# Kernel optimization log

Measured on AMD Instinct MI355X. Metric: run time of the kernel, lower is better.

## Reference

```python
import jax, jax.numpy as jnp
import numpy as np

D_ATT = 1024
N_HEADS = 16
D_HEAD = D_ATT // N_HEADS


def _xavier(key, shape, scale):
    # xavier_uniform for Linear(d, d): limit = sqrt(6/(fan_in+fan_out))
    limit = float(np.sqrt(6.0 / (shape[0] + shape[1])))
    return jax.random.uniform(key, shape, jnp.float32, -limit, limit) * scale


def setup_inputs() -> dict:
    key = jax.random.key(0)
    ks = jax.random.split(key, 7)
    B, Lt, Ls = 2, 2048, 2048
    s = 1.0 / np.sqrt(D_ATT)
    return {
        "x_target": jax.random.normal(ks[0], (B, Lt, D_ATT), jnp.float32),
        "x_source": jax.random.normal(ks[1], (B, Ls, D_ATT), jnp.float32),
        "Wq": _xavier(ks[2], (D_ATT, D_ATT), s),  # torch Linear weight [out, in]
        "Wk": _xavier(ks[3], (D_ATT, D_ATT), s),
        "Wv": _xavier(ks[4], (D_ATT, D_ATT), s),
        "Wo": _xavier(ks[5], (D_ATT, D_ATT), 1.0),
        "bo": jax.random.uniform(ks[6], (D_ATT,), jnp.float32, -s, s),
    }


def reference(x_target, x_source, Wq, Wk, Wv, Wo, bo):
    B, Lt, _ = x_target.shape
    Ls = x_source.shape[1]
    H, Dh = N_HEADS, D_HEAD
    # projections (torch Linear: x @ W^T); RoPE defaults to identity
    Q = (x_target @ Wq.T).reshape(B, Lt, H, Dh)  # [B, Lt, H, Dh]
    K = (x_source @ Wk.T).reshape(B, Ls, H, Dh)
    V = (x_source @ Wv.T).reshape(B, Ls, H, Dh)
    scores = jnp.einsum("bthd,bshd->bhts", Q, K) / np.sqrt(Dh)
    attn = jax.nn.softmax(scores, axis=-1)
    out = jnp.einsum("bhts,bshd->bthd", attn, V).reshape(B, Lt, H * Dh)
    return out @ Wo.T + bo  # dropout p=0 -> identity
```

## Files before the change

kernel.cpp:

```cpp
#include <hip/hip_runtime.h>
#include <hip/hip_bf16.h>

typedef short bf16x8 __attribute__((ext_vector_type(8)));
typedef float f32x4 __attribute__((ext_vector_type(4)));
typedef unsigned int uint2v __attribute__((ext_vector_type(2)));

__device__ __forceinline__ float bf2f(ushort u) {
    union { unsigned int i; float f; } v; v.i = ((unsigned int)u) << 16; return v.f;
}
__device__ __forceinline__ ushort f2bf(float f) {
    union { float f; unsigned int i; } v; v.f = f;
    unsigned int x = v.i;
    x += 0x7fffu + ((x >> 16) & 1u);
    return (ushort)(x >> 16);
}

#define MFMA(a, b, c) __builtin_amdgcn_mfma_f32_16x16x32_bf16(a, b, c, 0, 0, 0)

#define WAIT_BARRIER(N) asm volatile("s_waitcnt vmcnt(" #N ")\n\ts_barrier" ::: "memory")

__device__ __forceinline__ void gld_lds16(const ushort* g, ushort* l) {
    __builtin_amdgcn_global_load_lds(
        (const __attribute__((address_space(1))) unsigned int*)g,
        (__attribute__((address_space(3))) unsigned int*)l, 16, 0, 0);
}

#define WS_XT 0
#define WS_XS 4194304
#define WS_WQ 8388608
#define WS_WK 9437184
#define WS_WV 10485760
#define WS_WO 11534336
#define WS_QH 12582912
#define WS_KH 16777216
#define WS_VT 20971520
#define WS_AO 0

__global__ __launch_bounds__(256) void cast_bf16(
    const float* __restrict__ s0, const float* __restrict__ s1,
    const float* __restrict__ s2, const float* __restrict__ s3,
    const float* __restrict__ s4, const float* __restrict__ s5,
    ushort* __restrict__ ws)
{
    const int seg = blockIdx.y;
    const float* src = seg == 0 ? s0 : seg == 1 ? s1 : seg == 2 ? s2
                     : seg == 3 ? s3 : seg == 4 ? s4 : s5;
    const size_t off = seg == 0 ? WS_XT : seg == 1 ? WS_XS : seg == 2 ? WS_WQ
                     : seg == 3 ? WS_WK : seg == 4 ? WS_WV : (size_t)WS_WO;
    const int n4 = (seg < 2) ? 1048576 : 262144;
    const float scl = (seg == 2) ? 0.18033688f : 1.0f;
    ushort* d = ws + off;
    for (int i = blockIdx.x * 256 + threadIdx.x; i < n4; i += gridDim.x * 256) {
        float4 f = ((const float4*)src)[i];
        ushort4 u;
        u.x = f2bf(f.x * scl); u.y = f2bf(f.y * scl);
        u.z = f2bf(f.z * scl); u.w = f2bf(f.w * scl);
        ((ushort4*)d)[i] = u;
    }
}

__global__ __launch_bounds__(256) void gemm128(
    const ushort* __restrict__ xtb, const ushort* __restrict__ xsb,
    const ushort* __restrict__ wqb, const ushort* __restrict__ wkb,
    const ushort* __restrict__ wvb,
    ushort* __restrict__ qh, ushort* __restrict__ kh, ushort* __restrict__ vt)
{
    __shared__ __align__(16) ushort SM[24576];

    const int mode = blockIdx.z;
    const ushort* Ap = (mode == 0) ? xtb : xsb;
    const ushort* Wp = (mode == 0) ? wqb : (mode == 1 ? wkb : wvb);

    const int tid  = threadIdx.x;
    const int wave = tid >> 6, lane = tid & 63;
    const int quad = lane >> 4, lidx = lane & 15;
    const int wm = wave >> 1, wn = wave & 1;
    const int id = blockIdx.x + 8 * blockIdx.y;
    const int m0 = (id & 31) * 128, n0 = (id >> 5) * 128;

    const int slr = lane >> 2, scb = lane & 3;
    auto stage = [&](int k0, int bufi) {
        ushort* Asb = SM + bufi * 4096;
        ushort* Bsb = SM + 12288 + bufi * 4096;
#pragma unroll
        for (int i2 = 0; i2 < 2; ++i2) {
            const int i = wave + i2 * 4;
            const int r = i * 16 + slr;
            gld_lds16(Ap + (size_t)(m0 + r) * 1024 + k0 + scb * 8, Asb + i * 512);
            gld_lds16(Wp + (size_t)(n0 + r) * 1024 + k0 + scb * 8, Bsb + i * 512);
        }
    };

    f32x4 acc[4][4] = {};
    stage(0, 0);
    stage(32, 1);

    for (int kt = 0; kt < 32; ++kt) {
        const int cur = kt % 3;
        WAIT_BARRIER(4);
        stage(((kt + 2) & 31) * 32, (kt + 2) % 3);
        const ushort* Asb = SM + cur * 4096;
        const ushort* Bsb = SM + 12288 + cur * 4096;
        bf16x8 af[4], bfr[4];
#pragma unroll
        for (int i = 0; i < 4; ++i) {
            af[i]  = *(const bf16x8*)(Asb + (wm * 64 + i * 16 + lidx) * 32 + quad * 8);
            bfr[i] = *(const bf16x8*)(Bsb + (wn * 64 + i * 16 + lidx) * 32 + quad * 8);
        }
#pragma unroll
        for (int mi = 0; mi < 4; ++mi)
#pragma unroll
            for (int ni = 0; ni < 4; ++ni)
                acc[mi][ni] = MFMA(af[mi], bfr[ni], acc[mi][ni]);
    }
    __syncthreads();

    ushort* scr = SM + wave * 4096;

    if (mode == 2) {
#pragma unroll
        for (int mi = 0; mi < 4; ++mi)
#pragma unroll
            for (int ni = 0; ni < 4; ++ni)
#pragma unroll
                for (int r = 0; r < 4; ++r) {
                    const int dl = ni * 16 + lidx;
                    const int tl = mi * 16 + quad * 4 + r;
                    const int col = (((tl >> 3) ^ (dl & 7)) << 3) | (tl & 7);
                    scr[dl * 64 + col] = f2bf(acc[mi][ni][r]);
                }
        asm volatile("s_waitcnt lgkmcnt(0)" ::: "memory");
        const int hh = (n0 + wn * 64) >> 6;
        const int bb = m0 >> 11;
        const int t0 = (m0 + wm * 64) & 2047;
        ushort* Vtp = vt + (size_t)(bb * 16 + hh) * 64 * 2048;
#pragma unroll
        for (int ii = 0; ii < 8; ++ii) {
            const int dl = ii * 8 + (lane >> 3);
            const int tb = lane & 7;
            uint4 vd = *(const uint4*)(scr + dl * 64 + ((tb ^ (dl & 7)) << 3));
            *(uint4*)(Vtp + (size_t)dl * 2048 + t0 + tb * 8) = vd;
        }
        return;
    }

#pragma unroll
    for (int mi = 0; mi < 4; ++mi)
#pragma unroll
        for (int ni = 0; ni < 4; ++ni)
#pragma unroll
            for (int r = 0; r < 4; ++r) {
                const int tl = mi * 16 + quad * 4 + r;
                const int dl = ni * 16 + lidx;
                const int col = (((dl >> 3) ^ (tl & 7)) << 3) | (dl & 7);
                scr[tl * 64 + col] = f2bf(acc[mi][ni][r]);
            }
    asm volatile("s_waitcnt lgkmcnt(0)" ::: "memory");
    {
        ushort* dst = (mode == 0) ? qh : kh;
        const int hh = (n0 + wn * 64) >> 6;
        const int bb = m0 >> 11;
        const int tbase = (m0 + wm * 64) & 2047;
        ushort* Hp = dst + (size_t)(bb * 16 + hh) * 2048 * 64;
#pragma unroll
        for (int ii = 0; ii < 8; ++ii) {
            const int tl = ii * 8 + (lane >> 3);
            const int c  = lane & 7;
            uint4 vd = *(const uint4*)(scr + tl * 64 + ((c ^ (tl & 7)) << 3));
            *(uint4*)(Hp + (size_t)(tbase + tl) * 64 + c * 8) = vd;
        }
    }
}

__global__ __launch_bounds__(256) void gemm_out(
    const ushort* __restrict__ aob, const ushort* __restrict__ wob,
    const float* __restrict__ bias, float* __restrict__ outf)
{
    __shared__ __align__(16) ushort SM[18432];

    const int tid  = threadIdx.x;
    const int wave = tid >> 6, lane = tid & 63;
    const int quad = lane >> 4, lidx = lane & 15;
    const int id = blockIdx.x + 16 * blockIdx.y;
    const int m0 = (id & 31) * 128, n0 = (id >> 5) * 64;

    const int slr = lane >> 2, scb = lane & 3;
    auto stage = [&](int k0, int bufi) {
        ushort* Asb = SM + bufi * 4096;
        ushort* Bsb = SM + 12288 + bufi * 2048;
#pragma unroll
        for (int i2 = 0; i2 < 2; ++i2) {
            const int i = wave * 2 + i2;
            gld_lds16(aob + (size_t)(m0 + i * 16 + slr) * 1024 + k0 + scb * 8,
                      Asb + i * 512);
        }
        gld_lds16(wob + (size_t)(n0 + wave * 16 + slr) * 1024 + k0 + scb * 8,
                  Bsb + wave * 512);
    };

    f32x4 acc[2][4] = {};
    stage(0, 0);
    stage(32, 1);

    for (int kt = 0; kt < 32; ++kt) {
        const int cur = kt % 3;
        WAIT_BARRIER(3);
        stage(((kt + 2) & 31) * 32, (kt + 2) % 3);
        const ushort* Asb = SM + cur * 4096;
        const ushort* Bsb = SM + 12288 + cur * 2048;
        bf16x8 af[2], bfr[4];
#pragma unroll
        for (int i = 0; i < 2; ++i)
            af[i] = *(const bf16x8*)(Asb + (wave * 32 + i * 16 + lidx) * 32 + quad * 8);
#pragma unroll
        for (int i = 0; i < 4; ++i)
            bfr[i] = *(const bf16x8*)(Bsb + (i * 16 + lidx) * 32 + quad * 8);
#pragma unroll
        for (int mi = 0; mi < 2; ++mi)
#pragma unroll
            for (int ni = 0; ni < 4; ++ni)
                acc[mi][ni] = MFMA(af[mi], bfr[ni], acc[mi][ni]);
    }

#pragma unroll
    for (int mi = 0; mi < 2; ++mi)
#pragma unroll
        for (int ni = 0; ni < 4; ++ni)
#pragma unroll
            for (int r = 0; r < 4; ++r) {
                const int m = m0 + wave * 32 + mi * 16 + quad * 4 + r;
                const int n = n0 + ni * 16 + lidx;
                outf[(size_t)m * 1024 + n] = acc[mi][ni][r] + bias[n];
            }
}

__global__ __launch_bounds__(512, 6) void flash_attn(
    const ushort* __restrict__ Qh, const ushort* __restrict__ Kh,
    const ushort* __restrict__ Vt, ushort* __restrict__ AO)
{
    __shared__ __align__(16) ushort Kb[3][4096];
    __shared__ __align__(16) ushort Vb[3][4096];

    const int tid  = threadIdx.x;
    const int wave = tid >> 6, lane = tid & 63;
    const int quad = lane >> 4, lidx = lane & 15;
    const int bh = blockIdx.y;
    const int b = bh >> 4, h = bh & 15;
    const int qbase = blockIdx.x * 128 + wave * 16;

    const ushort* Qp = Qh + (size_t)bh * 2048 * 64;
    const ushort* Kp = Kh + (size_t)bh * 2048 * 64;
    const ushort* Vp = Vt + (size_t)bh * 64 * 2048;

    bf16x8 q0, q1;
    {
        const ushort* qr = Qp + (size_t)(qbase + lidx) * 64 + quad * 8;
        q0 = *(const bf16x8*)qr;
        q1 = *(const bf16x8*)(qr + 32);
    }

    auto stage = [&](int s0, int bufi) {
        const int slot = wave * 64 + lane;
        const int r  = slot >> 3;
        const int bb = slot & 7;
        const int gb = bb ^ (r & 7);
        gld_lds16(Kp + (size_t)(s0 + r) * 64 + gb * 8, &Kb[bufi][wave * 512]);
        gld_lds16(Vp + (size_t)r * 2048 + s0 + gb * 8, &Vb[bufi][wave * 512]);
    };

    auto swap2 = [&](uint& x, uint& y) {
        uint2v r1 = __builtin_amdgcn_permlane32_swap(x, y, false, false);
        uint2v r2 = __builtin_amdgcn_permlane16_swap(r1[0], r1[1], false, false);
        x = r2[0]; y = r2[1];
    };

    float lsum = 0.f;
    f32x4 o[4] = {};

    stage(0, 0);
    stage(64, 1);

    for (int j = 0; j < 32; ++j) {
        const int cur = j % 3;
        WAIT_BARRIER(2);
        stage(((j + 2) & 31) * 64, (j + 2) % 3);

        f32x4 s[4] = {};
#pragma unroll
        for (int n0 = 0; n0 < 4; ++n0) {
            const int row = n0 * 16 + lidx;
            bf16x8 kA = *(const bf16x8*)&Kb[cur][row * 64 + ((quad ^ (row & 7)) * 8)];
            bf16x8 kB = *(const bf16x8*)&Kb[cur][row * 64 + (((4 + quad) ^ (row & 7)) * 8)];
            s[n0] = MFMA(kA, q0, s[n0]);
            s[n0] = MFMA(kB, q1, s[n0]);
        }

        bf16x8 v0[4], v1[4];
#pragma unroll
        for (int n0 = 0; n0 < 4; ++n0) {
            const int d = n0 * 16 + lidx;
            v0[n0] = *(const bf16x8*)&Vb[cur][d * 64 + ((quad ^ (d & 7)) * 8)];
            v1[n0] = *(const bf16x8*)&Vb[cur][d * 64 + (((4 + quad) ^ (d & 7)) * 8)];
        }

        uint W[4][2];
#pragma unroll
        for (int n0 = 0; n0 < 4; ++n0) {
            float p0 = __builtin_amdgcn_exp2f(s[n0][0]);
            float p1 = __builtin_amdgcn_exp2f(s[n0][1]);
            float p2 = __builtin_amdgcn_exp2f(s[n0][2]);
            float p3 = __builtin_amdgcn_exp2f(s[n0][3]);
            lsum += (p0 + p1) + (p2 + p3);
            asm("v_cvt_pk_bf16_f32 %0, %1, %2" : "=v"(W[n0][0]) : "v"(p0), "v"(p1));
            asm("v_cvt_pk_bf16_f32 %0, %1, %2" : "=v"(W[n0][1]) : "v"(p2), "v"(p3));
        }

        uint aw0 = W[0][0], aw2 = W[1][0]; swap2(aw0, aw2);
        uint aw1 = W[0][1], aw3 = W[1][1]; swap2(aw1, aw3);
        uint bw0 = W[2][0], bw2 = W[3][0]; swap2(bw0, bw2);
        uint bw1 = W[2][1], bw3 = W[3][1]; swap2(bw1, bw3);
        union { uint u[4]; bf16x8 v; } PA, PB;
        PA.u[0] = aw0; PA.u[1] = aw1; PA.u[2] = aw2; PA.u[3] = aw3;
        PB.u[0] = bw0; PB.u[1] = bw1; PB.u[2] = bw2; PB.u[3] = bw3;

#pragma unroll
        for (int n0 = 0; n0 < 4; ++n0) {
            o[n0] = MFMA(PA.v, v0[n0], o[n0]);
            o[n0] = MFMA(PB.v, v1[n0], o[n0]);
        }
    }

    {
        float v = lsum;
        v += __shfl_xor(v, 16);
        v += __shfl_xor(v, 32);
        lsum = v;
    }
    float rs[4];
#pragma unroll
    for (int r = 0; r < 4; ++r)
        rs[r] = 1.0f / __shfl(lsum, quad * 4 + r);

#pragma unroll
    for (int n0 = 0; n0 < 4; ++n0)
#pragma unroll
        for (int r = 0; r < 4; ++r) {
            const int tt = qbase + quad * 4 + r;
            const int d  = n0 * 16 + lidx;
            AO[(size_t)(b * 2048 + tt) * 1024 + h * 64 + d] =
                f2bf(o[n0][r] * rs[r]);
        }
}

extern "C" void kernel_launch(void* const* d_in, const int* in_sizes, int n_in,
                              void* d_out, int out_size, void* d_ws, size_t ws_size,
                              hipStream_t stream) {
    const float* xt = (const float*)d_in[0];
    const float* xs = (const float*)d_in[1];
    const float* Wq = (const float*)d_in[2];
    const float* Wk = (const float*)d_in[3];
    const float* Wv = (const float*)d_in[4];
    const float* Wo = (const float*)d_in[5];
    const float* bo = (const float*)d_in[6];
    float* out = (float*)d_out;

    ushort* ws = (ushort*)d_ws;

    cast_bf16<<<dim3(1024, 6, 1), 256, 0, stream>>>(xt, xs, Wq, Wk, Wv, Wo, ws);

    gemm128<<<dim3(8, 32, 3), 256, 0, stream>>>(
        ws + WS_XT, ws + WS_XS, ws + WS_WQ, ws + WS_WK, ws + WS_WV,
        ws + WS_QH, ws + WS_KH, ws + WS_VT);

    flash_attn<<<dim3(16, 32, 1), 512, 0, stream>>>(
        ws + WS_QH, ws + WS_KH, ws + WS_VT, ws + WS_AO);

    gemm_out<<<dim3(16, 32, 1), 256, 0, stream>>>(
        ws + WS_AO, ws + WS_WO, bo, out);
}
```

Baseline: 190.3 us.

## Fuse K and V projections into one block sharing the x_source tile

The QKV projection kernel now runs two grid planes instead of three. The K plane also loads Wv tiles and keeps a second accumulator set, so each x_source tile is loaded once and used for both the K and V GEMMs. This removes the redundant x_source global reads and one third of the blocks. In exchange, the fused blocks carry twice the accumulators and more shared memory, which may lower occupancy. The work is also uneven between the Q blocks and the fused K/V blocks.

Measured after the change: 198.4 us. 4.2% more time.

```diff
diff --git a/kernel.cpp b/kernel.cpp
--- a/kernel.cpp
+++ b/kernel.cpp
@@ -65,11 +65,11 @@
     const ushort* __restrict__ wvb,
     ushort* __restrict__ qh, ushort* __restrict__ kh, ushort* __restrict__ vt)
 {
-    __shared__ __align__(16) ushort SM[24576];
+    __shared__ __align__(16) ushort SM[36864];
 
     const int mode = blockIdx.z;
-    const ushort* Ap = (mode == 0) ? xtb : xsb;
-    const ushort* Wp = (mode == 0) ? wqb : (mode == 1 ? wkb : wvb);
+    const ushort* Ap = mode ? xsb : xtb;
+    const ushort* Bkp = mode ? wkb : wqb;
 
     const int tid  = threadIdx.x;
     const int wave = tid >> 6, lane = tid & 63;
@@ -81,43 +81,89 @@
     const int slr = lane >> 2, scb = lane & 3;
     auto stage = [&](int k0, int bufi) {
         ushort* Asb = SM + bufi * 4096;
-        ushort* Bsb = SM + 12288 + bufi * 4096;
+        ushort* Bksb = SM + 12288 + bufi * 4096;
+        ushort* Bvsb = SM + 24576 + bufi * 4096;
 #pragma unroll
         for (int i2 = 0; i2 < 2; ++i2) {
             const int i = wave + i2 * 4;
             const int r = i * 16 + slr;
             gld_lds16(Ap + (size_t)(m0 + r) * 1024 + k0 + scb * 8, Asb + i * 512);
-            gld_lds16(Wp + (size_t)(n0 + r) * 1024 + k0 + scb * 8, Bsb + i * 512);
+            gld_lds16(Bkp + (size_t)(n0 + r) * 1024 + k0 + scb * 8, Bksb + i * 512);
+            if (mode)
+                gld_lds16(wvb + (size_t)(n0 + r) * 1024 + k0 + scb * 8,
+                          Bvsb + i * 512);
         }
     };
 
-    f32x4 acc[4][4] = {};
+    f32x4 aK[4][4] = {};
+    f32x4 aV[4][4] = {};
     stage(0, 0);
     stage(32, 1);
 
     for (int kt = 0; kt < 32; ++kt) {
         const int cur = kt % 3;
-        WAIT_BARRIER(4);
+        if (mode) { WAIT_BARRIER(6); } else { WAIT_BARRIER(4); }
         stage(((kt + 2) & 31) * 32, (kt + 2) % 3);
         const ushort* Asb = SM + cur * 4096;
-        const ushort* Bsb = SM + 12288 + cur * 4096;
-        bf16x8 af[4], bfr[4];
+        const ushort* Bksb = SM + 12288 + cur * 4096;
+        const ushort* Bvsb = SM + 24576 + cur * 4096;
+        bf16x8 af[4], bk[4];
 #pragma unroll
         for (int i = 0; i < 4; ++i) {
-            af[i]  = *(const bf16x8*)(Asb + (wm * 64 + i * 16 + lidx) * 32 + quad * 8);
-            bfr[i] = *(const bf16x8*)(Bsb + (wn * 64 + i * 16 + lidx) * 32 + quad * 8);
+            af[i] = *(const bf16x8*)(Asb + (wm * 64 + i * 16 + lidx) * 32 + quad * 8);
+            bk[i] = *(const bf16x8*)(Bksb + (wn * 64 + i * 16 + lidx) * 32 + quad * 8);
         }
 #pragma unroll
         for (int mi = 0; mi < 4; ++mi)
 #pragma unroll
             for (int ni = 0; ni < 4; ++ni)
-                acc[mi][ni] = MFMA(af[mi], bfr[ni], acc[mi][ni]);
+                aK[mi][ni] = MFMA(af[mi], bk[ni], aK[mi][ni]);
+        if (mode) {
+            bf16x8 bv[4];
+#pragma unroll
+            for (int i = 0; i < 4; ++i)
+                bv[i] = *(const bf16x8*)(Bvsb + (wn * 64 + i * 16 + lidx) * 32 + quad * 8);
+#pragma unroll
+            for (int mi = 0; mi < 4; ++mi)
+#pragma unroll
+                for (int ni = 0; ni < 4; ++ni)
+                    aV[mi][ni] = MFMA(af[mi], bv[ni], aV[mi][ni]);
+        }
     }
     __syncthreads();
 
     ushort* scr = SM + wave * 4096;
-
-    if (mode == 2) {
+    const int hh = (n0 + wn * 64) >> 6;
+    const int bb = m0 >> 11;
+
+    {
+#pragma unroll
+        for (int mi = 0; mi < 4; ++mi)
+#pragma unroll
+            for (int ni = 0; ni < 4; ++ni)
+#pragma unroll
+                for (int r = 0; r < 4; ++r) {
+                    const int tl = mi * 16 + quad * 4 + r;
+                    const int dl = ni * 16 + lidx;
+                    const int col = (((dl >> 3) ^ (tl & 7)) << 3) | (dl & 7);
+                    scr[tl * 64 + col] = f2bf(aK[mi][ni][r]);
+                }
+        asm volatile("s_waitcnt lgkmcnt(0)" ::: "memory");
+        ushort* dst = mode ? kh : qh;
+        const int tbase = (m0 + wm * 64) & 2047;
+        ushort* Hp = dst + (size_t)(bb * 16 + hh) * 2048 * 64;
+#pragma unroll
+        for (int ii = 0; ii < 8; ++ii) {
+            const int tl = ii * 8 + (lane >> 3);
+            const int c  = lane & 7;
+            uint4 vd = *(const uint4*)(scr + tl * 64 + ((c ^ (tl & 7)) << 3));
+            *(uint4*)(Hp + (size_t)(tbase + tl) * 64 + c * 8) = vd;
+        }
+    }
+
+    if (!mode) return;
+
+    {
 #pragma unroll
         for (int mi = 0; mi < 4; ++mi)
 #pragma unroll
@@ -127,11 +173,9 @@
                     const int dl = ni * 16 + lidx;
                     const int tl = mi * 16 + quad * 4 + r;
                     const int col = (((tl >> 3) ^ (dl & 7)) << 3) | (tl & 7);
-                    scr[dl * 64 + col] = f2bf(acc[mi][ni][r]);
+                    scr[dl * 64 + col] = f2bf(aV[mi][ni][r]);
                 }
         asm volatile("s_waitcnt lgkmcnt(0)" ::: "memory");
-        const int hh = (n0 + wn * 64) >> 6;
-        const int bb = m0 >> 11;
         const int t0 = (m0 + wm * 64) & 2047;
         ushort* Vtp = vt + (size_t)(bb * 16 + hh) * 64 * 2048;
 #pragma unroll
@@ -140,34 +184,6 @@
             const int tb = lane & 7;
             uint4 vd = *(const uint4*)(scr + dl * 64 + ((tb ^ (dl & 7)) << 3));
             *(uint4*)(Vtp + (size_t)dl * 2048 + t0 + tb * 8) = vd;
-        }
-        return;
-    }
-
-#pragma unroll
-    for (int mi = 0; mi < 4; ++mi)
-#pragma unroll
-        for (int ni = 0; ni < 4; ++ni)
-#pragma unroll
-            for (int r = 0; r < 4; ++r) {
-                const int tl = mi * 16 + quad * 4 + r;
-                const int dl = ni * 16 + lidx;
-                const int col = (((dl >> 3) ^ (tl & 7)) << 3) | (dl & 7);
-                scr[tl * 64 + col] = f2bf(acc[mi][ni][r]);
-            }
-    asm volatile("s_waitcnt lgkmcnt(0)" ::: "memory");
-    {
-        ushort* dst = (mode == 0) ? qh : kh;
-        const int hh = (n0 + wn * 64) >> 6;
-        const int bb = m0 >> 11;
-        const int tbase = (m0 + wm * 64) & 2047;
-        ushort* Hp = dst + (size_t)(bb * 16 + hh) * 2048 * 64;
-#pragma unroll
-        for (int ii = 0; ii < 8; ++ii) {
-            const int tl = ii * 8 + (lane >> 3);
-            const int c  = lane & 7;
-            uint4 vd = *(const uint4*)(scr + tl * 64 + ((c ^ (tl & 7)) << 3));
-            *(uint4*)(Hp + (size_t)(tbase + tl) * 64 + c * 8) = vd;
         }
     }
 }
@@ -368,7 +384,7 @@
 
     cast_bf16<<<dim3(1024, 6, 1), 256, 0, stream>>>(xt, xs, Wq, Wk, Wv, Wo, ws);
 
-    gemm128<<<dim3(8, 32, 3), 256, 0, stream>>>(
+    gemm128<<<dim3(8, 32, 2), 256, 0, stream>>>(
         ws + WS_XT, ws + WS_XS, ws + WS_WQ, ws + WS_WK, ws + WS_WV,
         ws + WS_QH, ws + WS_KH, ws + WS_VT);
 
```
